# Performance work log

Hardware: AMD Instinct MI355X
Metric: run time of the kernel (lower is better)

Reference implementation:

```python
import jax, jax.numpy as jnp
import numpy as np

N = 100_000   # nodes
E = 1_600_000 # edges
F = 16        # input node features
H = 32        # embedding_size
B = 256       # graphs in batch


def setup_inputs() -> dict:
    key = jax.random.key(0)
    ks = jax.random.split(key, 13)
    s = 0.1  # small init scale for weights
    return {
        "x": jax.random.normal(ks[0], (N, F), jnp.float32),
        "edge_index": jax.random.randint(ks[1], (2, E), 0, N, dtype=jnp.int64),
        "batch_index": jnp.sort(jax.random.randint(ks[2], (N,), 0, B, dtype=jnp.int64)),
        "W0": jax.random.normal(ks[3], (F, H), jnp.float32) * s,
        "b0": jax.random.normal(ks[4], (H,), jnp.float32) * s,
        "W1": jax.random.normal(ks[5], (H, H), jnp.float32) * s,
        "b1": jax.random.normal(ks[6], (H,), jnp.float32) * s,
        "W2": jax.random.normal(ks[7], (H, H), jnp.float32) * s,
        "b2": jax.random.normal(ks[8], (H,), jnp.float32) * s,
        "W3": jax.random.normal(ks[9], (H, H), jnp.float32) * s,
        "b3": jax.random.normal(ks[10], (H, H), jnp.float32)[:, 0] * s,
        "W_out": jax.random.normal(ks[11], (3 * H, 1), jnp.float32) * s,
        "b_out": jax.random.normal(ks[12], (1,), jnp.float32) * s,
    }


def _gcn_forward(x, edge_index, batch_index,
                 W0, b0, W1, b1, W2, b2, W3, b3, W_out, b_out):
    src, dst = edge_index[0], edge_index[1]
    n = x.shape[0]
    # GCN symmetric normalization with self-loops: deg includes the +1 self-loop
    deg = jax.ops.segment_sum(jnp.ones(src.shape[0], x.dtype), dst, num_segments=n) + 1.0
    dinv = jax.lax.rsqrt(deg)
    edge_coef = (dinv[src] * dinv[dst])[:, None]   # [E,1]
    self_coef = (dinv * dinv)[:, None]             # [N,1]

    def conv(h, W, b):
        # x' = D^{-1/2}(A+I)D^{-1/2} (h W) + b  (PyG GCNConv)
        hW = h @ W
        agg = jax.ops.segment_sum(hW[src] * edge_coef, dst, num_segments=n)
        agg = agg + hW * self_coef  # self-loop contribution
        return agg + b

    h = jnp.tanh(conv(x, W0, b0))
    h = jnp.tanh(conv(h, W1, b1))
    h = jnp.tanh(conv(h, W2, b2))
    h = jnp.tanh(conv(h, W3, b3))

    # Global max / mean / add pooling over batch_index
    gmax = jax.ops.segment_max(h, batch_index, num_segments=B)
    gsum = jax.ops.segment_sum(h, batch_index, num_segments=B)
    cnt = jax.ops.segment_sum(jnp.ones(n, h.dtype), batch_index, num_segments=B)
    gmean = gsum / jnp.maximum(cnt, 1.0)[:, None]
    pooled = jnp.concatenate([gmax, gmean, gsum], axis=1)  # [B, 3H]

    out = pooled @ W_out + b_out  # [B, 1]
    return out, pooled


def reference(x, edge_index, batch_index,
              W0, b0, W1, b1, W2, b2, W3, b3, W_out, b_out):
    return _gcn_forward(x, edge_index, batch_index,
                        W0, b0, W1, b1, W2, b2, W3, b3, W_out, b_out)
```

## Files before the change

kernel.cpp:

```cpp
#include <hip/hip_runtime.h>
#include <math.h>

#define N_NODES 100000
#define N_EDGES 1600000
#define F_IN    16
#define H_DIM   32
#define B_GRAPHS 256

#define BSHIFT  7
#define BSIZE   128
#define NBUCKET ((N_NODES + BSIZE - 1) / BSIZE)
#define EPB     8192
#define NCHUNK  ((N_EDGES + EPB - 1) / EPB)
#define CAP     4096
#define PADR    (BSIZE * 7)
#define TPAD    (N_EDGES + NBUCKET * PADR)
#define NPB     16
#define LAYER_BLOCKS (N_NODES / NPB)

__device__ inline float bf_lo(unsigned u) { return __uint_as_float(u << 16); }
__device__ inline float bf_hi(unsigned u) { return __uint_as_float(u & 0xffff0000u); }
__device__ inline unsigned pack_bf16x2(float a, float b) {
    unsigned ua = __float_as_uint(a), ub = __float_as_uint(b);
    ua += 0x7fffu + ((ua >> 16) & 1u);
    ub += 0x7fffu + ((ub >> 16) & 1u);
    return (ua >> 16) | (ub & 0xffff0000u);
}

__global__ __launch_bounds__(256) void passA_kernel(const int* __restrict__ dst,
                                                    int* __restrict__ bucket_cnt) {
    __shared__ int hist[NBUCKET];
    int t = threadIdx.x;
    for (int k = t; k < NBUCKET; k += 256) hist[k] = 0;
    __syncthreads();
    int base = blockIdx.x * EPB;
    int end  = base + EPB; if (end > N_EDGES) end = N_EDGES;
    for (int e = base + t; e < end; e += 256) atomicAdd(&hist[dst[e] >> BSHIFT], 1);
    __syncthreads();
    for (int k = t; k < NBUCKET; k += 256)
        if (hist[k]) atomicAdd(&bucket_cnt[k], hist[k]);
}

__global__ __launch_bounds__(256) void scan_kernel(const int* __restrict__ bucket_cnt,
                                                   int* __restrict__ bucket_off,
                                                   int* __restrict__ bucket_cur) {
    __shared__ int s[1024];
    int t = threadIdx.x;
    int v[4];
    for (int r = 0; r < 4; ++r) {
        int k = t + 256 * r;
        int x = (k < NBUCKET) ? bucket_cnt[k] : 0;
        v[r] = x; s[k] = x;
    }
    __syncthreads();
    for (int off = 1; off < 1024; off <<= 1) {
        int tmp[4];
        for (int r = 0; r < 4; ++r) { int k = t + 256 * r; tmp[r] = (k >= off) ? s[k - off] : 0; }
        __syncthreads();
        for (int r = 0; r < 4; ++r) { int k = t + 256 * r; s[k] += tmp[r]; }
        __syncthreads();
    }
    for (int r = 0; r < 4; ++r) {
        int k = t + 256 * r;
        if (k < NBUCKET) {
            int excl = s[k] - v[r];
            bucket_off[k] = excl;
            bucket_cur[k] = excl;
        }
    }
    if (t == 0) bucket_off[NBUCKET] = s[1023];
}

__global__ __launch_bounds__(256) void passB_kernel(const int* __restrict__ ei,
                                                    int* __restrict__ bucket_cur,
                                                    unsigned* __restrict__ rec_out) {
    __shared__ int hist[NBUCKET];
    __shared__ int sbase[NBUCKET];
    __shared__ int gbase[NBUCKET];
    __shared__ int scnt[NBUCKET];
    __shared__ int ssc[1024];
    __shared__ unsigned stage[EPB];
    int t = threadIdx.x;
    for (int k = t; k < NBUCKET; k += 256) { hist[k] = 0; scnt[k] = 0; }
    __syncthreads();

    const int* dst = ei + N_EDGES;
    int base = blockIdx.x * EPB;
    int end  = base + EPB; if (end > N_EDGES) end = N_EDGES;

    for (int e = base + t; e < end; e += 256) atomicAdd(&hist[dst[e] >> BSHIFT], 1);
    __syncthreads();

    int v[4];
    for (int r = 0; r < 4; ++r) {
        int k = t + 256 * r;
        int x = (k < NBUCKET) ? hist[k] : 0;
        v[r] = x; ssc[k] = x;
    }
    __syncthreads();
    for (int off = 1; off < 1024; off <<= 1) {
        int tmp[4];
        for (int r = 0; r < 4; ++r) { int k = t + 256 * r; tmp[r] = (k >= off) ? ssc[k - off] : 0; }
        __syncthreads();
        for (int r = 0; r < 4; ++r) { int k = t + 256 * r; ssc[k] += tmp[r]; }
        __syncthreads();
    }
    for (int r = 0; r < 4; ++r) {
        int k = t + 256 * r;
        if (k < NBUCKET) sbase[k] = ssc[k] - v[r];
    }
    for (int k = t; k < NBUCKET; k += 256) {
        int h = hist[k];
        gbase[k] = h ? atomicAdd(&bucket_cur[k], h) : 0;
    }
    __syncthreads();

    for (int e = base + t; e < end; e += 256) {
        int d = dst[e], s = ei[e];
        int bk = d >> BSHIFT;
        int off = atomicAdd(&scnt[bk], 1);
        stage[sbase[bk] + off] = (unsigned)s | ((unsigned)(d & (BSIZE - 1)) << 20);
    }
    __syncthreads();

    int wave = t >> 6, lane = t & 63;
    for (int bk = wave; bk < NBUCKET; bk += 4) {
        int h = hist[bk];
        if (h == 0) continue;
        int sb = sbase[bk], gb = gbase[bk];
        for (int j = lane; j < h; j += 64)
            rec_out[gb + j] = stage[sb + j];
    }
}

__global__ __launch_bounds__(256) void dinv_kernel(const unsigned* __restrict__ rec,
                                                   const int* __restrict__ bucket_off,
                                                   float* __restrict__ dinv) {
    __shared__ int cnt[BSIZE];
    int t = threadIdx.x, b = blockIdx.x;
    if (t < BSIZE) cnt[t] = 0;
    __syncthreads();
    int e1 = bucket_off[b + 1];
    for (int e = bucket_off[b] + t; e < e1; e += 256) atomicAdd(&cnt[rec[e] >> 20], 1);
    __syncthreads();
    int nd = (b << BSHIFT) + t;
    if (t < BSIZE && nd < N_NODES) dinv[nd] = rsqrtf((float)cnt[t] + 1.0f);
}

__global__ __launch_bounds__(256) void passC_kernel(const unsigned* __restrict__ rec,
                                                    const int* __restrict__ bucket_off,
                                                    const float* __restrict__ dinv,
                                                    int2* __restrict__ row_meta,
                                                    int* __restrict__ csr_src,
                                                    float* __restrict__ csr_coef) {
    __shared__ unsigned stage[CAP];
    __shared__ int cnt[BSIZE];
    __shared__ int pds[BSIZE];
    __shared__ int cur[BSIZE];
    __shared__ float sdv[BSIZE];
    int t = threadIdx.x, b = blockIdx.x;
    int node0 = b << BSHIFT;
    int e0 = bucket_off[b], e1 = bucket_off[b + 1];
    int n = e1 - e0;
    int pbase = e0 + b * PADR;
    if (t < BSIZE) {
        cnt[t] = 0;
        int nd = node0 + t;
        sdv[t] = (nd < N_NODES) ? dinv[nd] : 0.f;
    }
    __syncthreads();
    for (int k = t; k < n; k += 256) {
        unsigned r = rec[e0 + k];
        stage[k] = r;
        atomicAdd(&cnt[r >> 20], 1);
    }
    __syncthreads();
    int pd = 0;
    if (t < BSIZE) { pd = (cnt[t] + 7) & ~7; pds[t] = pd; }
    __syncthreads();
    for (int off = 1; off < BSIZE; off <<= 1) {
        int v = (t < BSIZE && t >= off) ? pds[t - off] : 0;
        __syncthreads();
        if (t < BSIZE) pds[t] += v;
        __syncthreads();
    }
    if (t < BSIZE) {
        int startp = pbase + pds[t] - pd;
        cur[t] = startp;
        int nd = node0 + t;
        if (nd < N_NODES) row_meta[nd] = make_int2(startp, pd);
        for (int k = startp + cnt[t]; k < startp + pd; ++k) {
            csr_src[k]  = 0;
            csr_coef[k] = 0.f;
        }
    }
    __syncthreads();
    for (int k = t; k < n; k += 256) {
        unsigned r = stage[k];
        int dl = r >> 20;
        int s  = r & 0xFFFFF;
        int pos = atomicAdd(&cur[dl], 1);
        csr_src[pos]  = s;
        csr_coef[pos] = dinv[s] * sdv[dl];
    }
}

template <int FIN, bool PACKED>
__global__ __launch_bounds__(256) void layer_kernel(
        const void* __restrict__ h_in_v,
        const int2* __restrict__ row_meta,
        const int* __restrict__ csr_src,
        const float* __restrict__ csr_coef,
        const float* __restrict__ dinv,
        const float* __restrict__ W,
        const float* __restrict__ bias,
        unsigned* __restrict__ h_out) {
    constexpr int STR = FIN + 1;
    __shared__ float sW[FIN * H_DIM];
    __shared__ float sb[H_DIM];
    __shared__ float agg[NPB][STR];
    int t = threadIdx.x;
    for (int k = t; k < FIN * H_DIM; k += 256) sW[k] = W[k];
    if (t < H_DIM) sb[t] = bias[t];

    int nl = t >> 4, ln = t & 15;
    int i = blockIdx.x * NPB + nl;
    int2 m = row_meta[i];
    float di = dinv[i], di2 = di * di;
    int eend = m.x + m.y;

    if (PACKED) {
        const unsigned* hp = (const unsigned*)h_in_v;
        unsigned u = hp[i * 16 + ln];
        float acc0 = bf_lo(u) * di2, acc1 = bf_hi(u) * di2;
        for (int e = m.x; e < eend; e += 8) {
            int s[8]; float c[8]; unsigned v[8];
#pragma unroll
            for (int k = 0; k < 8; ++k) { s[k] = csr_src[e + k]; c[k] = csr_coef[e + k]; }
#pragma unroll
            for (int k = 0; k < 8; ++k) v[k] = hp[s[k] * 16 + ln];
#pragma unroll
            for (int k = 0; k < 8; ++k) { acc0 += bf_lo(v[k]) * c[k]; acc1 += bf_hi(v[k]) * c[k]; }
        }
        agg[nl][2 * ln]     = acc0;
        agg[nl][2 * ln + 1] = acc1;
    } else {
        const float* xf = (const float*)h_in_v;
        float acc = xf[i * F_IN + ln] * di2;
        for (int e = m.x; e < eend; e += 8) {
            int s[8]; float c[8]; float v[8];
#pragma unroll
            for (int k = 0; k < 8; ++k) { s[k] = csr_src[e + k]; c[k] = csr_coef[e + k]; }
#pragma unroll
            for (int k = 0; k < 8; ++k) v[k] = xf[s[k] * F_IN + ln];
#pragma unroll
            for (int k = 0; k < 8; ++k) acc += v[k] * c[k];
        }
        agg[nl][ln] = acc;
    }
    __syncthreads();

    int j0 = 2 * ln;
    float o0 = sb[j0], o1 = sb[j0 + 1];
    const float* arow = &agg[nl][0];
#pragma unroll
    for (int k = 0; k < FIN; ++k) {
        float a = arow[k];
        o0 += a * sW[k * H_DIM + j0];
        o1 += a * sW[k * H_DIM + j0 + 1];
    }
    h_out[i * 16 + ln] = pack_bf16x2(tanhf(o0), tanhf(o1));
}

__global__ __launch_bounds__(256) void pool_kernel(const unsigned* __restrict__ hp,
                                                   const int* __restrict__ batch,
                                                   const float* __restrict__ Wout,
                                                   const float* __restrict__ bout,
                                                   float* __restrict__ out) {
    int b = blockIdx.x;
    int t = threadIdx.x;
    int lane_n = t >> 5;
    int j = t & 31;

    int lo = 0, hi = N_NODES;
    while (lo < hi) { int mid = (lo + hi) >> 1; if (batch[mid] < b) lo = mid + 1; else hi = mid; }
    int start = lo;
    hi = N_NODES;
    while (lo < hi) { int mid = (lo + hi) >> 1; if (batch[mid] < b + 1) lo = mid + 1; else hi = mid; }
    int end = lo;

    float vmax = -INFINITY, vsum = 0.f;
    for (int i = start + lane_n; i < end; i += 8) {
        unsigned q = hp[i * 16 + (j >> 1)];
        float v = (j & 1) ? bf_hi(q) : bf_lo(q);
        vmax = fmaxf(vmax, v);
        vsum += v;
    }

    __shared__ float smax[8][32];
    __shared__ float ssum[8][32];
    __shared__ float pool96[96];
    smax[lane_n][j] = vmax;
    ssum[lane_n][j] = vsum;
    __syncthreads();

    if (t < 32) {
        float m = smax[0][t], s = ssum[0][t];
#pragma unroll
        for (int n = 1; n < 8; ++n) { m = fmaxf(m, smax[n][t]); s += ssum[n][t]; }
        int cnt = end - start;
        float mean = s / fmaxf((float)cnt, 1.0f);
        pool96[t]      = m;
        pool96[32 + t] = mean;
        pool96[64 + t] = s;
    }
    __syncthreads();

    if (t < 96) out[B_GRAPHS + b * 96 + t] = pool96[t];

    __shared__ float dotbuf[96];
    if (t < 96) dotbuf[t] = pool96[t] * Wout[t];
    __syncthreads();
    if (t == 0) {
        float acc = 0.f;
#pragma unroll
        for (int k = 0; k < 96; ++k) acc += dotbuf[k];
        out[b] = acc + bout[0];
    }
}

extern "C" void kernel_launch(void* const* d_in, const int* in_sizes, int n_in,
                              void* d_out, int out_size, void* d_ws, size_t ws_size,
                              hipStream_t stream) {
    const float* x     = (const float*)d_in[0];
    const int*   ei    = (const int*)  d_in[1];
    const int*   batch = (const int*)  d_in[2];
    const float* W0    = (const float*)d_in[3];
    const float* b0    = (const float*)d_in[4];
    const float* W1    = (const float*)d_in[5];
    const float* b1    = (const float*)d_in[6];
    const float* W2    = (const float*)d_in[7];
    const float* b2    = (const float*)d_in[8];
    const float* W3    = (const float*)d_in[9];
    const float* b3    = (const float*)d_in[10];
    const float* Wout  = (const float*)d_in[11];
    const float* bout  = (const float*)d_in[12];
    float* out = (float*)d_out;

    char* p = (char*)d_ws;
    float*    dinv       = (float*)p;    p += (size_t)N_NODES * 4;
    unsigned* hA         = (unsigned*)p; p += (size_t)N_NODES * 16 * 4;
    unsigned* rec        = (unsigned*)p; p += (size_t)N_EDGES * 4;
    int*      csr_src    = (int*)p;      p += (size_t)TPAD * 4;
    float*    csr_coef   = (float*)p;    p += (size_t)TPAD * 4;
    int2*     row_meta   = (int2*)p;     p += (size_t)N_NODES * 8;
    int*      bucket_cnt = (int*)p;      p += NBUCKET * 4;
    int*      bucket_off = (int*)p;      p += (NBUCKET + 1) * 4;
    int*      bucket_cur = (int*)p;      p += NBUCKET * 4;
    unsigned* hB = rec;

    hipMemsetAsync(bucket_cnt, 0, NBUCKET * sizeof(int), stream);
    passA_kernel<<<NCHUNK, 256, 0, stream>>>(ei + N_EDGES, bucket_cnt);
    scan_kernel<<<1, 256, 0, stream>>>(bucket_cnt, bucket_off, bucket_cur);
    passB_kernel<<<NCHUNK, 256, 0, stream>>>(ei, bucket_cur, rec);
    dinv_kernel<<<NBUCKET, 256, 0, stream>>>(rec, bucket_off, dinv);
    passC_kernel<<<NBUCKET, 256, 0, stream>>>(rec, bucket_off, dinv,
                                              row_meta, csr_src, csr_coef);

    layer_kernel<F_IN, false><<<LAYER_BLOCKS, 256, 0, stream>>>(
        x,  row_meta, csr_src, csr_coef, dinv, W0, b0, hA);
    layer_kernel<H_DIM, true><<<LAYER_BLOCKS, 256, 0, stream>>>(
        hA, row_meta, csr_src, csr_coef, dinv, W1, b1, hB);
    layer_kernel<H_DIM, true><<<LAYER_BLOCKS, 256, 0, stream>>>(
        hB, row_meta, csr_src, csr_coef, dinv, W2, b2, hA);
    layer_kernel<H_DIM, true><<<LAYER_BLOCKS, 256, 0, stream>>>(
        hA, row_meta, csr_src, csr_coef, dinv, W3, b3, hB);

    pool_kernel<<<B_GRAPHS, 256, 0, stream>>>(hB, batch, Wout, bout, out);
}
```

Measured before the change: 316.1 us.

## Interleave CSR src/coef into int2 pairs and simplify passB scatter

Merges the separate csr_src and csr_coef arrays into one interleaved int2 array, so each layer kernel reads edge index and coefficient together with 16-byte int4 loads. The bucket base is aligned to 8 entries so the vector loads stay aligned. passB drops its shared-memory staging, local scan and coalesced copy-out, and instead scatters records straight to global memory through per-bucket shared atomic cursors. The scatter writes are less coalesced, and the interleaved layout raises the workspace for the CSR arrays' padding slightly.

Result: faster. 277.9 us (-12.1%).

```diff
diff --git a/kernel.cpp b/kernel.cpp
--- a/kernel.cpp
+++ b/kernel.cpp
@@ -13,8 +13,8 @@
 #define EPB     8192
 #define NCHUNK  ((N_EDGES + EPB - 1) / EPB)
 #define CAP     4096
-#define PADR    (BSIZE * 7)
-#define TPAD    (N_EDGES + NBUCKET * PADR)
+#define PADR2   904
+#define TPAD    (N_EDGES + NBUCKET * PADR2)
 #define NPB     16
 #define LAYER_BLOCKS (N_NODES / NPB)
 
@@ -75,13 +75,9 @@
                                                     int* __restrict__ bucket_cur,
                                                     unsigned* __restrict__ rec_out) {
     __shared__ int hist[NBUCKET];
-    __shared__ int sbase[NBUCKET];
-    __shared__ int gbase[NBUCKET];
-    __shared__ int scnt[NBUCKET];
-    __shared__ int ssc[1024];
-    __shared__ unsigned stage[EPB];
-    int t = threadIdx.x;
-    for (int k = t; k < NBUCKET; k += 256) { hist[k] = 0; scnt[k] = 0; }
+    __shared__ int gcur[NBUCKET];
+    int t = threadIdx.x;
+    for (int k = t; k < NBUCKET; k += 256) hist[k] = 0;
     __syncthreads();
 
     const int* dst = ei + N_EDGES;
@@ -91,45 +87,17 @@
     for (int e = base + t; e < end; e += 256) atomicAdd(&hist[dst[e] >> BSHIFT], 1);
     __syncthreads();
 
-    int v[4];
-    for (int r = 0; r < 4; ++r) {
-        int k = t + 256 * r;
-        int x = (k < NBUCKET) ? hist[k] : 0;
-        v[r] = x; ssc[k] = x;
-    }
-    __syncthreads();
-    for (int off = 1; off < 1024; off <<= 1) {
-        int tmp[4];
-        for (int r = 0; r < 4; ++r) { int k = t + 256 * r; tmp[r] = (k >= off) ? ssc[k - off] : 0; }
-        __syncthreads();
-        for (int r = 0; r < 4; ++r) { int k = t + 256 * r; ssc[k] += tmp[r]; }
-        __syncthreads();
-    }
-    for (int r = 0; r < 4; ++r) {
-        int k = t + 256 * r;
-        if (k < NBUCKET) sbase[k] = ssc[k] - v[r];
-    }
     for (int k = t; k < NBUCKET; k += 256) {
         int h = hist[k];
-        gbase[k] = h ? atomicAdd(&bucket_cur[k], h) : 0;
+        gcur[k] = h ? atomicAdd(&bucket_cur[k], h) : 0;
     }
     __syncthreads();
 
     for (int e = base + t; e < end; e += 256) {
         int d = dst[e], s = ei[e];
         int bk = d >> BSHIFT;
-        int off = atomicAdd(&scnt[bk], 1);
-        stage[sbase[bk] + off] = (unsigned)s | ((unsigned)(d & (BSIZE - 1)) << 20);
-    }
-    __syncthreads();
-
-    int wave = t >> 6, lane = t & 63;
-    for (int bk = wave; bk < NBUCKET; bk += 4) {
-        int h = hist[bk];
-        if (h == 0) continue;
-        int sb = sbase[bk], gb = gbase[bk];
-        for (int j = lane; j < h; j += 64)
-            rec_out[gb + j] = stage[sb + j];
+        int pos = atomicAdd(&gcur[bk], 1);
+        rec_out[pos] = (unsigned)s | ((unsigned)(d & (BSIZE - 1)) << 20);
     }
 }
 
@@ -151,8 +119,8 @@
                                                     const int* __restrict__ bucket_off,
                                                     const float* __restrict__ dinv,
                                                     int2* __restrict__ row_meta,
-                                                    int* __restrict__ csr_src,
-                                                    float* __restrict__ csr_coef) {
+                                                    int2* __restrict__ csr,
+                                                    const int* __restrict__ dummy_unused) {
     __shared__ unsigned stage[CAP];
     __shared__ int cnt[BSIZE];
     __shared__ int pds[BSIZE];
@@ -162,7 +130,7 @@
     int node0 = b << BSHIFT;
     int e0 = bucket_off[b], e1 = bucket_off[b + 1];
     int n = e1 - e0;
-    int pbase = e0 + b * PADR;
+    int pbase = (e0 + b * PADR2 + 7) & ~7;
     if (t < BSIZE) {
         cnt[t] = 0;
         int nd = node0 + t;
@@ -189,10 +157,8 @@
         cur[t] = startp;
         int nd = node0 + t;
         if (nd < N_NODES) row_meta[nd] = make_int2(startp, pd);
-        for (int k = startp + cnt[t]; k < startp + pd; ++k) {
-            csr_src[k]  = 0;
-            csr_coef[k] = 0.f;
-        }
+        for (int k = startp + cnt[t]; k < startp + pd; ++k)
+            csr[k] = make_int2(0, 0);
     }
     __syncthreads();
     for (int k = t; k < n; k += 256) {
@@ -200,8 +166,7 @@
         int dl = r >> 20;
         int s  = r & 0xFFFFF;
         int pos = atomicAdd(&cur[dl], 1);
-        csr_src[pos]  = s;
-        csr_coef[pos] = dinv[s] * sdv[dl];
+        csr[pos] = make_int2(s, __float_as_int(dinv[s] * sdv[dl]));
     }
 }
 
@@ -209,8 +174,7 @@
 __global__ __launch_bounds__(256) void layer_kernel(
         const void* __restrict__ h_in_v,
         const int2* __restrict__ row_meta,
-        const int* __restrict__ csr_src,
-        const float* __restrict__ csr_coef,
+        const int4* __restrict__ csr4,
         const float* __restrict__ dinv,
         const float* __restrict__ W,
         const float* __restrict__ bias,
@@ -227,34 +191,43 @@
     int i = blockIdx.x * NPB + nl;
     int2 m = row_meta[i];
     float di = dinv[i], di2 = di * di;
-    int eend = m.x + m.y;
+    int p0i = m.x >> 1;
+    int p1i = (m.x + m.y) >> 1;
 
     if (PACKED) {
         const unsigned* hp = (const unsigned*)h_in_v;
         unsigned u = hp[i * 16 + ln];
         float acc0 = bf_lo(u) * di2, acc1 = bf_hi(u) * di2;
-        for (int e = m.x; e < eend; e += 8) {
-            int s[8]; float c[8]; unsigned v[8];
-#pragma unroll
-            for (int k = 0; k < 8; ++k) { s[k] = csr_src[e + k]; c[k] = csr_coef[e + k]; }
-#pragma unroll
-            for (int k = 0; k < 8; ++k) v[k] = hp[s[k] * 16 + ln];
-#pragma unroll
-            for (int k = 0; k < 8; ++k) { acc0 += bf_lo(v[k]) * c[k]; acc1 += bf_hi(v[k]) * c[k]; }
+        for (int q = p0i; q < p1i; q += 4) {
+            int4 a = csr4[q], b = csr4[q + 1], c = csr4[q + 2], d = csr4[q + 3];
+            unsigned v0 = hp[a.x * 16 + ln], v1 = hp[a.z * 16 + ln];
+            unsigned v2 = hp[b.x * 16 + ln], v3 = hp[b.z * 16 + ln];
+            unsigned v4 = hp[c.x * 16 + ln], v5 = hp[c.z * 16 + ln];
+            unsigned v6 = hp[d.x * 16 + ln], v7 = hp[d.z * 16 + ln];
+            float c0 = __int_as_float(a.y), c1 = __int_as_float(a.w);
+            float c2 = __int_as_float(b.y), c3 = __int_as_float(b.w);
+            float c4 = __int_as_float(c.y), c5 = __int_as_float(c.w);
+            float c6 = __int_as_float(d.y), c7 = __int_as_float(d.w);
+            acc0 += bf_lo(v0) * c0 + bf_lo(v1) * c1 + bf_lo(v2) * c2 + bf_lo(v3) * c3
+                  + bf_lo(v4) * c4 + bf_lo(v5) * c5 + bf_lo(v6) * c6 + bf_lo(v7) * c7;
+            acc1 += bf_hi(v0) * c0 + bf_hi(v1) * c1 + bf_hi(v2) * c2 + bf_hi(v3) * c3
+                  + bf_hi(v4) * c4 + bf_hi(v5) * c5 + bf_hi(v6) * c6 + bf_hi(v7) * c7;
         }
         agg[nl][2 * ln]     = acc0;
         agg[nl][2 * ln + 1] = acc1;
     } else {
         const float* xf = (const float*)h_in_v;
         float acc = xf[i * F_IN + ln] * di2;
-        for (int e = m.x; e < eend; e += 8) {
-            int s[8]; float c[8]; float v[8];
-#pragma unroll
-            for (int k = 0; k < 8; ++k) { s[k] = csr_src[e + k]; c[k] = csr_coef[e + k]; }
-#pragma unroll
-            for (int k = 0; k < 8; ++k) v[k] = xf[s[k] * F_IN + ln];
-#pragma unroll
-            for (int k = 0; k < 8; ++k) acc += v[k] * c[k];
+        for (int q = p0i; q < p1i; q += 4) {
+            int4 a = csr4[q], b = csr4[q + 1], c = csr4[q + 2], d = csr4[q + 3];
+            float v0 = xf[a.x * F_IN + ln], v1 = xf[a.z * F_IN + ln];
+            float v2 = xf[b.x * F_IN + ln], v3 = xf[b.z * F_IN + ln];
+            float v4 = xf[c.x * F_IN + ln], v5 = xf[c.z * F_IN + ln];
+            float v6 = xf[d.x * F_IN + ln], v7 = xf[d.z * F_IN + ln];
+            acc += v0 * __int_as_float(a.y) + v1 * __int_as_float(a.w)
+                 + v2 * __int_as_float(b.y) + v3 * __int_as_float(b.w)
+                 + v4 * __int_as_float(c.y) + v5 * __int_as_float(c.w)
+                 + v6 * __int_as_float(d.y) + v7 * __int_as_float(d.w);
         }
         agg[nl][ln] = acc;
     }
@@ -351,8 +324,7 @@
     float*    dinv       = (float*)p;    p += (size_t)N_NODES * 4;
     unsigned* hA         = (unsigned*)p; p += (size_t)N_NODES * 16 * 4;
     unsigned* rec        = (unsigned*)p; p += (size_t)N_EDGES * 4;
-    int*      csr_src    = (int*)p;      p += (size_t)TPAD * 4;
-    float*    csr_coef   = (float*)p;    p += (size_t)TPAD * 4;
+    int2*     csr        = (int2*)p;     p += (size_t)TPAD * 8;
     int2*     row_meta   = (int2*)p;     p += (size_t)N_NODES * 8;
     int*      bucket_cnt = (int*)p;      p += NBUCKET * 4;
     int*      bucket_off = (int*)p;      p += (NBUCKET + 1) * 4;
@@ -365,16 +337,16 @@
     passB_kernel<<<NCHUNK, 256, 0, stream>>>(ei, bucket_cur, rec);
     dinv_kernel<<<NBUCKET, 256, 0, stream>>>(rec, bucket_off, dinv);
     passC_kernel<<<NBUCKET, 256, 0, stream>>>(rec, bucket_off, dinv,
-                                              row_meta, csr_src, csr_coef);
+                                              row_meta, csr, (const int*)nullptr);
 
     layer_kernel<F_IN, false><<<LAYER_BLOCKS, 256, 0, stream>>>(
-        x,  row_meta, csr_src, csr_coef, dinv, W0, b0, hA);
+        x,  row_meta, (const int4*)csr, dinv, W0, b0, hA);
     layer_kernel<H_DIM, true><<<LAYER_BLOCKS, 256, 0, stream>>>(
-        hA, row_meta, csr_src, csr_coef, dinv, W1, b1, hB);
+        hA, row_meta, (const int4*)csr, dinv, W1, b1, hB);
     layer_kernel<H_DIM, true><<<LAYER_BLOCKS, 256, 0, stream>>>(
-        hB, row_meta, csr_src, csr_coef, dinv, W2, b2, hA);
+        hB, row_meta, (const int4*)csr, dinv, W2, b2, hA);
     layer_kernel<H_DIM, true><<<LAYER_BLOCKS, 256, 0, stream>>>(
-        hA, row_meta, csr_src, csr_coef, dinv, W3, b3, hB);
+        hA, row_meta, (const int4*)csr, dinv, W3, b3, hB);
 
     pool_kernel<<<B_GRAPHS, 256, 0, stream>>>(hB, batch, Wout, bout, out);
 }
```
